# Optimization experiments

Hardware: AMD Instinct MI355X
Metric: run time of the kernel (lower is better)

The kernel has to match this reference:

```python
import jax, jax.numpy as jnp
import numpy as np

B, S, D = 4, 1024, 1024      # batch, seq_len, hidden_size
I = 4096                     # intermediate_size
E = 8                        # num_experts
K = 2                        # top-k


def setup_inputs() -> dict:
    key = jax.random.key(0)
    ks = jax.random.split(key, 8)
    x = jax.random.normal(ks[0], (B, S, D), dtype=jnp.float32)
    gate_w = jax.random.normal(ks[1], (E, D), dtype=jnp.float32) * 0.02
    gate_b = jnp.zeros((E,), dtype=jnp.float32)
    w1 = jax.random.normal(ks[2], (E, I, D), dtype=jnp.float32) * 0.02
    b1 = jnp.zeros((E, I), dtype=jnp.float32)
    w2 = jax.random.normal(ks[3], (E, D, I), dtype=jnp.float32) * 0.02
    b2 = jnp.zeros((E, D), dtype=jnp.float32)
    return {"x": x, "gate_w": gate_w, "gate_b": gate_b,
            "w1": w1, "b1": b1, "w2": w2, "b2": b2}


def reference(x, gate_w, gate_b, w1, b1, w2, b2):
    b, s, d = x.shape
    xf = x.reshape(-1, d)                                  # [N, D]
    logits = xf @ gate_w.T + gate_b                        # [N, E]
    top_vals, top_idx = jax.lax.top_k(logits, K)           # [N, K]
    top_w = jax.nn.softmax(top_vals, axis=-1)              # softmax over the k selected logits

    # combine[n, e] = routing weight of token n for expert e (0 if not selected)
    n_tok = xf.shape[0]
    combine = jnp.zeros((n_tok, w1.shape[0]), dtype=x.dtype)
    combine = combine.at[jnp.arange(n_tok)[:, None], top_idx].add(top_w)

    out = jnp.zeros_like(xf)
    for e in range(w1.shape[0]):                           # small fixed loop over experts
        h = jax.nn.gelu(xf @ w1[e].T + b1[e], approximate=False)  # exact GELU (torch default)
        out = out + combine[:, e:e + 1] * (h @ w2[e].T + b2[e])
    return out.reshape(b, s, d)
```

## Files before the change

### kernel.cpp

```cpp
#include <hip/hip_runtime.h>
#include <math.h>

#define NTOK 4096
#define DDIM 1024
#define IDIM 4096
#define NEXP 8
#define MAXPAD 9216

typedef _Float16 f16x8 __attribute__((ext_vector_type(8)));
typedef _Float16 f16x4 __attribute__((ext_vector_type(4)));
typedef float    f32x4 __attribute__((ext_vector_type(4)));

__device__ __forceinline__ void glds16(const _Float16* g, _Float16* l) {
    __builtin_amdgcn_global_load_lds(
        (const __attribute__((address_space(1))) _Float16*)g,
        (__attribute__((address_space(3))) _Float16*)l, 16, 0, 0);
}

__device__ __forceinline__ float fast_gelu(float v) {
    float u = v * (0.7978845608f + 0.0356774081f * v * v);
    float ex = __builtin_amdgcn_exp2f(u * 2.8853900817779268f);
    float th = 1.0f - 2.0f * __builtin_amdgcn_rcpf(ex + 1.0f);
    return 0.5f * v * (1.0f + th);
}

__global__ void cvt_kernel(const float* __restrict__ src, _Float16* __restrict__ dst, int n4) {
    int i = blockIdx.x * blockDim.x + threadIdx.x;
    if (i >= n4) return;
    float4 v = ((const float4*)src)[i];
    f16x4 o = { (_Float16)v.x, (_Float16)v.y, (_Float16)v.z, (_Float16)v.w };
    ((f16x4*)dst)[i] = o;
}

__global__ void gate_kernel(const float* __restrict__ x, const float* __restrict__ gw,
                            const float* __restrict__ gb,
                            int* __restrict__ cnt, int* __restrict__ tok,
                            float* __restrict__ wgt) {
    int wave = threadIdx.x >> 6;
    int lane = threadIdx.x & 63;
    int token = blockIdx.x * 4 + wave;
    const float* xr = x + (size_t)token * DDIM;
    float xv[16];
#pragma unroll
    for (int j = 0; j < 16; ++j) xv[j] = xr[lane + 64 * j];
    float lg[NEXP];
#pragma unroll
    for (int e = 0; e < NEXP; ++e) {
        const float* g = gw + e * DDIM;
        float s = 0.f;
#pragma unroll
        for (int j = 0; j < 16; ++j) s += xv[j] * g[lane + 64 * j];
#pragma unroll
        for (int o = 32; o > 0; o >>= 1) s += __shfl_xor(s, o, 64);
        lg[e] = s + gb[e];
    }
    if (lane == 0) {
        int i0 = 0; float v0 = lg[0];
        for (int e = 1; e < NEXP; ++e) if (lg[e] > v0) { v0 = lg[e]; i0 = e; }
        int i1 = -1; float v1 = -3.0e38f;
        for (int e = 0; e < NEXP; ++e) { if (e == i0) continue; if (lg[e] > v1) { v1 = lg[e]; i1 = e; } }
        float e1 = expf(v1 - v0);
        float den = 1.f + e1;
        float w0 = 1.f / den;
        float w1 = e1 / den;
        int p0 = atomicAdd(&cnt[i0], 1);
        tok[i0 * NTOK + p0] = token; wgt[i0 * NTOK + p0] = w0;
        int p1 = atomicAdd(&cnt[i1], 1);
        tok[i1 * NTOK + p1] = token; wgt[i1 * NTOK + p1] = w1;
    }
}

__global__ void scan_kernel(const int* __restrict__ cnt, int* __restrict__ off,
                            int* __restrict__ q1, int* __restrict__ q2) {
    if (threadIdx.x == 0) {
        int acc = 0;
        for (int e = 0; e < NEXP; ++e) { off[e] = acc; acc += ((cnt[e] + 127) >> 7) << 7; }
        off[NEXP] = acc;
        int n1 = 0, n2 = 0;
        for (int e = 0; e < NEXP; ++e) {
            int mtiles = (cnt[e] + 255) >> 8;
            for (int mt = 0; mt < mtiles; ++mt) {
                for (int nt = 0; nt < IDIM / 256; ++nt)
                    q1[n1++] = e | (mt << 4) | (nt << 12);
                for (int kc = 0; kc < 4; ++kc)
                    for (int nt = 0; nt < DDIM / 256; ++nt)
                        q2[n2++] = e | (mt << 4) | (nt << 12) | (kc << 20);
            }
        }
        off[10] = n1; off[11] = n2;
    }
}

__global__ void gather_kernel(const float* __restrict__ x, const int* __restrict__ cnt,
                              const int* __restrict__ off, const int* __restrict__ tok,
                              _Float16* __restrict__ xg) {
    int row = blockIdx.x;
    if (row >= off[NEXP]) return;
    int e = 0;
    while (e < NEXP - 1 && row >= off[e + 1]) ++e;
    int r = row - off[e];
    int t = threadIdx.x;
    _Float16* dst = xg + (size_t)row * DDIM;
    if (r < cnt[e]) {
        int token = tok[e * NTOK + r];
        float4 v = ((const float4*)(x + (size_t)token * DDIM))[t];
        f16x4 o = { (_Float16)v.x, (_Float16)v.y, (_Float16)v.z, (_Float16)v.w };
        ((f16x4*)dst)[t] = o;
    } else {
        f16x4 z = {};
        ((f16x4*)dst)[t] = z;
    }
}

#define SBAR() do { __builtin_amdgcn_s_barrier(); asm volatile("" ::: "memory"); } while (0)
#define STAGE(b, ko) do { \
    glds16(ap + (ko), &As[b][wv * 512]); \
    glds16(bp + (ko), &Bs[b][wv * 512]); \
} while (0)
#define ARD(buf, r) (*(const f16x8*)&As[buf][(r) * 32 + ((fq ^ (((r) >> 1) & 3)) << 3)])
#define BRD(buf, r) (*(const f16x8*)&Bs[buf][(r) * 32 + ((fq ^ (((r) >> 1) & 3)) << 3)])

template <int KDIM, int NDIM, int EPI, int SPLIT>
__global__ __launch_bounds__(1024, 4) void gemm256_kernel(
    const _Float16* __restrict__ A,
    const _Float16* __restrict__ Bw,
    const float* __restrict__ bias,
    const int* __restrict__ cnt, const int* __restrict__ off,
    const int* __restrict__ tok, const float* __restrict__ wgt,
    _Float16* __restrict__ Hout, float* __restrict__ Out,
    const int* __restrict__ qarr, const int* __restrict__ qn) {
    constexpr int KB = KDIM / SPLIT;
    constexpr int NK = KB / 32;

    __shared__ __align__(16) _Float16 As[4][256 * 32];
    __shared__ __align__(16) _Float16 Bs[4][256 * 32];

    const int tid = threadIdx.x;
    const int wv = tid >> 6, lane = tid & 63;
    const int wm = (wv >> 2) * 64;
    const int wn = (wv & 3) * 64;
    const int fr = lane & 15, fq = lane >> 4;
    const int srow = lane >> 2;
    const int scol = ((lane & 3) ^ ((lane >> 3) & 3)) << 3;
    const int nwork = *qn;

    for (int wi = blockIdx.x; wi < nwork; wi += gridDim.x) {
        __syncthreads();
        const int w = qarr[wi];
        const int e  = w & 15;
        const int mt = (w >> 4) & 255;
        const int nt = (w >> 12) & 255;
        const int kc = (w >> 20) & 7;
        const int ce = cnt[e];
        const int rowbase = off[e] + mt * 256;
        const int colbase = nt * 256;

        int ra = rowbase + wv * 16 + srow;
        if (ra > MAXPAD - 1) ra = MAXPAD - 1;
        const _Float16* ap = A + (size_t)ra * KDIM + kc * KB + scol;
        const _Float16* bp = Bw + ((size_t)e * NDIM + colbase + wv * 16 + srow) * KDIM + kc * KB + scol;

        f32x4 acc[4][4] = {};

        STAGE(0, 0); STAGE(1, 32); STAGE(2, 64);

        for (int kt = 0; kt < NK; ++kt) {
            const int buf = kt & 3;
            if (kt + 3 < NK) STAGE((kt + 3) & 3, (kt + 3) * 32);
            const int ahead = (NK - 1 - kt) < 3 ? (NK - 1 - kt) : 3;
            if (ahead == 3)      asm volatile("s_waitcnt vmcnt(6)" ::: "memory");
            else if (ahead == 2) asm volatile("s_waitcnt vmcnt(4)" ::: "memory");
            else if (ahead == 1) asm volatile("s_waitcnt vmcnt(2)" ::: "memory");
            else                 asm volatile("s_waitcnt vmcnt(0)" ::: "memory");
            SBAR();
            f16x8 a[4], b[4];
#pragma unroll
            for (int i = 0; i < 4; ++i) a[i] = ARD(buf, wm + i * 16 + fr);
#pragma unroll
            for (int j = 0; j < 4; ++j) b[j] = BRD(buf, wn + j * 16 + fr);
            __builtin_amdgcn_s_setprio(1);
#pragma unroll
            for (int i = 0; i < 4; ++i)
#pragma unroll
                for (int j = 0; j < 4; ++j)
                    acc[i][j] = __builtin_amdgcn_mfma_f32_16x16x32_f16(a[i], b[j], acc[i][j], 0, 0, 0);
            __builtin_amdgcn_s_setprio(0);
            asm volatile("s_waitcnt lgkmcnt(0)" ::: "memory");
            SBAR();
        }

        const int rq = fq << 2;
        if constexpr (EPI == 1) {
            const int elim = off[e + 1];
#pragma unroll
            for (int i = 0; i < 4; ++i) {
#pragma unroll
                for (int r = 0; r < 4; ++r) {
                    const int grow = rowbase + wm + i * 16 + rq + r;
                    if (grow < elim) {
#pragma unroll
                        for (int j = 0; j < 4; ++j) {
                            const int col = colbase + wn + j * 16 + fr;
                            float v = fast_gelu(acc[i][j][r] + bias[e * NDIM + col]);
                            Hout[(size_t)grow * NDIM + col] = (_Float16)v;
                        }
                    }
                }
            }
        } else {
#pragma unroll
            for (int i = 0; i < 4; ++i) {
#pragma unroll
                for (int r = 0; r < 4; ++r) {
                    const int slot = mt * 256 + wm + i * 16 + rq + r;
                    if (slot < ce) {
                        const int token = tok[e * NTOK + slot];
                        const float ww = wgt[e * NTOK + slot];
#pragma unroll
                        for (int j = 0; j < 4; ++j) {
                            const int col = colbase + wn + j * 16 + fr;
                            float v = acc[i][j][r];
                            if (kc == 0) v += bias[e * NDIM + col];
                            unsafeAtomicAdd(&Out[(size_t)token * NDIM + col], ww * v);
                        }
                    }
                }
            }
        }
    }
}

extern "C" void kernel_launch(void* const* d_in, const int* in_sizes, int n_in,
                              void* d_out, int out_size, void* d_ws, size_t ws_size,
                              hipStream_t stream) {
    const float* x      = (const float*)d_in[0];
    const float* gate_w = (const float*)d_in[1];
    const float* gate_b = (const float*)d_in[2];
    const float* w1     = (const float*)d_in[3];
    const float* b1     = (const float*)d_in[4];
    const float* w2     = (const float*)d_in[5];
    const float* b2     = (const float*)d_in[6];
    float* out = (float*)d_out;

    char* p = (char*)d_ws;
    _Float16* w1h  = (_Float16*)p; p += (size_t)NEXP * IDIM * DDIM * 2;
    _Float16* w2h  = (_Float16*)p; p += (size_t)NEXP * DDIM * IDIM * 2;
    _Float16* xg   = (_Float16*)p; p += (size_t)MAXPAD * DDIM * 2;
    _Float16* hbuf = (_Float16*)p; p += (size_t)MAXPAD * IDIM * 2;
    int*      tok  = (int*)p;      p += (size_t)NEXP * NTOK * 4;
    float*    wgt  = (float*)p;    p += (size_t)NEXP * NTOK * 4;
    int*      cnt  = (int*)p;      p += 128;
    int*      off  = (int*)p;      p += 128;
    int*      q1   = (int*)p;      p += 4096;
    int*      q2   = (int*)p;      p += 4096;

    hipMemsetAsync(cnt, 0, 128, stream);
    hipMemsetAsync(out, 0, (size_t)NTOK * DDIM * 4, stream);

    cvt_kernel<<<32768, 256, 0, stream>>>(w2, w2h, NEXP * DDIM * IDIM / 4);
    cvt_kernel<<<32768, 256, 0, stream>>>(w1, w1h, NEXP * IDIM * DDIM / 4);
    gate_kernel<<<NTOK / 4, 256, 0, stream>>>(x, gate_w, gate_b, cnt, tok, wgt);
    scan_kernel<<<1, 64, 0, stream>>>(cnt, off, q1, q2);
    gather_kernel<<<MAXPAD, 256, 0, stream>>>(x, cnt, off, tok, xg);

    gemm256_kernel<DDIM, IDIM, 1, 1><<<dim3(256), 1024, 0, stream>>>(
        xg, w1h, b1, cnt, off, tok, wgt, hbuf, (float*)nullptr, q1, off + 10);
    gemm256_kernel<IDIM, DDIM, 2, 4><<<dim3(256), 1024, 0, stream>>>(
        hbuf, w2h, b2, cnt, off, tok, wgt, (_Float16*)nullptr, out, q2, off + 11);
}
```

Before: 781.0 us.

## Shrink GEMM tiles to 128x256 with 512-thread blocks and double buffering

```diff
diff --git a/kernel.cpp b/kernel.cpp
--- a/kernel.cpp
+++ b/kernel.cpp
@@ -78,7 +78,7 @@
         off[NEXP] = acc;
         int n1 = 0, n2 = 0;
         for (int e = 0; e < NEXP; ++e) {
-            int mtiles = (cnt[e] + 255) >> 8;
+            int mtiles = (cnt[e] + 127) >> 7;
             for (int mt = 0; mt < mtiles; ++mt) {
                 for (int nt = 0; nt < IDIM / 256; ++nt)
                     q1[n1++] = e | (mt << 4) | (nt << 12);
@@ -112,16 +112,16 @@
     }
 }
 
-#define SBAR() do { __builtin_amdgcn_s_barrier(); asm volatile("" ::: "memory"); } while (0)
 #define STAGE(b, ko) do { \
-    glds16(ap + (ko), &As[b][wv * 512]); \
-    glds16(bp + (ko), &Bs[b][wv * 512]); \
+    glds16(gp0 + (ko), &Sh[b][lo0]); \
+    glds16(gp1 + (ko), &Sh[b][lo1]); \
+    glds16(gp2 + (ko), &Sh[b][lo2]); \
 } while (0)
-#define ARD(buf, r) (*(const f16x8*)&As[buf][(r) * 32 + ((fq ^ (((r) >> 1) & 3)) << 3)])
-#define BRD(buf, r) (*(const f16x8*)&Bs[buf][(r) * 32 + ((fq ^ (((r) >> 1) & 3)) << 3)])
+#define ARD(buf, r) (*(const f16x8*)&Sh[buf][(r) * 32 + ((fq ^ (((r) >> 1) & 3)) << 3)])
+#define BRD(buf, r) (*(const f16x8*)&Sh[buf][4096 + (r) * 32 + ((fq ^ (((r) >> 1) & 3)) << 3)])
 
 template <int KDIM, int NDIM, int EPI, int SPLIT>
-__global__ __launch_bounds__(1024, 4) void gemm256_kernel(
+__global__ __launch_bounds__(512, 4) void gemm256_kernel(
     const _Float16* __restrict__ A,
     const _Float16* __restrict__ Bw,
     const float* __restrict__ bias,
@@ -132,8 +132,7 @@
     constexpr int KB = KDIM / SPLIT;
     constexpr int NK = KB / 32;
 
-    __shared__ __align__(16) _Float16 As[4][256 * 32];
-    __shared__ __align__(16) _Float16 Bs[4][256 * 32];
+    __shared__ __align__(16) _Float16 Sh[2][384 * 32];
 
     const int tid = threadIdx.x;
     const int wv = tid >> 6, lane = tid & 63;
@@ -148,36 +147,49 @@
         __syncthreads();
         const int w = qarr[wi];
         const int e  = w & 15;
-        const int mt = (w >> 4) & 255;
-        const int nt = (w >> 12) & 255;
+        const int mt = (w >> 4) & 63;
+        const int nt = (w >> 12) & 31;
         const int kc = (w >> 20) & 7;
         const int ce = cnt[e];
-        const int rowbase = off[e] + mt * 256;
+        const int rowbase = off[e] + mt * 128;
         const int colbase = nt * 256;
 
-        int ra = rowbase + wv * 16 + srow;
-        if (ra > MAXPAD - 1) ra = MAXPAD - 1;
-        const _Float16* ap = A + (size_t)ra * KDIM + kc * KB + scol;
-        const _Float16* bp = Bw + ((size_t)e * NDIM + colbase + wv * 16 + srow) * KDIM + kc * KB + scol;
+        const int id0 = wv * 3, id1 = wv * 3 + 1, id2 = wv * 3 + 2;
+        const _Float16* gp0; const _Float16* gp1; const _Float16* gp2;
+        int lo0, lo1, lo2;
+        {
+            const _Float16* Ab = A + (size_t)rowbase * KDIM + kc * KB + scol;
+            const _Float16* Bb = Bw + ((size_t)e * NDIM + colbase) * KDIM + kc * KB + scol;
+            gp0 = (id0 < 8) ? Ab + (size_t)(id0 * 16 + srow) * KDIM
+                            : Bb + (size_t)((id0 - 8) * 16 + srow) * KDIM;
+            gp1 = (id1 < 8) ? Ab + (size_t)(id1 * 16 + srow) * KDIM
+                            : Bb + (size_t)((id1 - 8) * 16 + srow) * KDIM;
+            gp2 = Bb + (size_t)((id2 - 8) * 16 + srow) * KDIM;
+            if (id2 < 8) gp2 = Ab + (size_t)(id2 * 16 + srow) * KDIM;
+            lo0 = (id0 < 8) ? id0 * 512 : 4096 + (id0 - 8) * 512;
+            lo1 = (id1 < 8) ? id1 * 512 : 4096 + (id1 - 8) * 512;
+            lo2 = (id2 < 8) ? id2 * 512 : 4096 + (id2 - 8) * 512;
+        }
 
         f32x4 acc[4][4] = {};
 
-        STAGE(0, 0); STAGE(1, 32); STAGE(2, 64);
+        STAGE(0, 0);
 
         for (int kt = 0; kt < NK; ++kt) {
-            const int buf = kt & 3;
-            if (kt + 3 < NK) STAGE((kt + 3) & 3, (kt + 3) * 32);
-            const int ahead = (NK - 1 - kt) < 3 ? (NK - 1 - kt) : 3;
-            if (ahead == 3)      asm volatile("s_waitcnt vmcnt(6)" ::: "memory");
-            else if (ahead == 2) asm volatile("s_waitcnt vmcnt(4)" ::: "memory");
-            else if (ahead == 1) asm volatile("s_waitcnt vmcnt(2)" ::: "memory");
-            else                 asm volatile("s_waitcnt vmcnt(0)" ::: "memory");
-            SBAR();
+            const int cur = kt & 1, nxt = cur ^ 1;
+            if (kt + 1 < NK) {
+                STAGE(nxt, (kt + 1) * 32);
+                asm volatile("s_waitcnt vmcnt(3)");
+            } else {
+                asm volatile("s_waitcnt vmcnt(0)");
+            }
+            __builtin_amdgcn_s_barrier();
+            __builtin_amdgcn_sched_barrier(0);
             f16x8 a[4], b[4];
 #pragma unroll
-            for (int i = 0; i < 4; ++i) a[i] = ARD(buf, wm + i * 16 + fr);
-#pragma unroll
-            for (int j = 0; j < 4; ++j) b[j] = BRD(buf, wn + j * 16 + fr);
+            for (int i = 0; i < 4; ++i) a[i] = ARD(cur, wm + i * 16 + fr);
+#pragma unroll
+            for (int j = 0; j < 4; ++j) b[j] = BRD(cur, wn + j * 16 + fr);
             __builtin_amdgcn_s_setprio(1);
 #pragma unroll
             for (int i = 0; i < 4; ++i)
@@ -185,25 +197,23 @@
                 for (int j = 0; j < 4; ++j)
                     acc[i][j] = __builtin_amdgcn_mfma_f32_16x16x32_f16(a[i], b[j], acc[i][j], 0, 0, 0);
             __builtin_amdgcn_s_setprio(0);
-            asm volatile("s_waitcnt lgkmcnt(0)" ::: "memory");
-            SBAR();
+            __builtin_amdgcn_sched_barrier(0);
+            asm volatile("s_waitcnt lgkmcnt(0)");
+            __builtin_amdgcn_s_barrier();
         }
 
         const int rq = fq << 2;
         if constexpr (EPI == 1) {
-            const int elim = off[e + 1];
 #pragma unroll
             for (int i = 0; i < 4; ++i) {
 #pragma unroll
                 for (int r = 0; r < 4; ++r) {
                     const int grow = rowbase + wm + i * 16 + rq + r;
-                    if (grow < elim) {
-#pragma unroll
-                        for (int j = 0; j < 4; ++j) {
-                            const int col = colbase + wn + j * 16 + fr;
-                            float v = fast_gelu(acc[i][j][r] + bias[e * NDIM + col]);
-                            Hout[(size_t)grow * NDIM + col] = (_Float16)v;
-                        }
+#pragma unroll
+                    for (int j = 0; j < 4; ++j) {
+                        const int col = colbase + wn + j * 16 + fr;
+                        float v = fast_gelu(acc[i][j][r] + bias[e * NDIM + col]);
+                        Hout[(size_t)grow * NDIM + col] = (_Float16)v;
                     }
                 }
             }
@@ -212,7 +222,7 @@
             for (int i = 0; i < 4; ++i) {
 #pragma unroll
                 for (int r = 0; r < 4; ++r) {
-                    const int slot = mt * 256 + wm + i * 16 + rq + r;
+                    const int slot = mt * 128 + wm + i * 16 + rq + r;
                     if (slot < ce) {
                         const int token = tok[e * NTOK + slot];
                         const float ww = wgt[e * NTOK + slot];
@@ -251,8 +261,8 @@
     float*    wgt  = (float*)p;    p += (size_t)NEXP * NTOK * 4;
     int*      cnt  = (int*)p;      p += 128;
     int*      off  = (int*)p;      p += 128;
-    int*      q1   = (int*)p;      p += 4096;
-    int*      q2   = (int*)p;      p += 4096;
+    int*      q1   = (int*)p;      p += 8192;
+    int*      q2   = (int*)p;      p += 8192;
 
     hipMemsetAsync(cnt, 0, 128, stream);
     hipMemsetAsync(out, 0, (size_t)NTOK * DDIM * 4, stream);
@@ -263,8 +273,8 @@
     scan_kernel<<<1, 64, 0, stream>>>(cnt, off, q1, q2);
     gather_kernel<<<MAXPAD, 256, 0, stream>>>(x, cnt, off, tok, xg);
 
-    gemm256_kernel<DDIM, IDIM, 1, 1><<<dim3(256), 1024, 0, stream>>>(
+    gemm256_kernel<DDIM, IDIM, 1, 1><<<dim3(512), 512, 0, stream>>>(
         xg, w1h, b1, cnt, off, tok, wgt, hbuf, (float*)nullptr, q1, off + 10);
-    gemm256_kernel<IDIM, DDIM, 2, 4><<<dim3(256), 1024, 0, stream>>>(
+    gemm256_kernel<IDIM, DDIM, 2, 4><<<dim3(512), 512, 0, stream>>>(
         hbuf, w2h, b2, cnt, off, tok, wgt, (_Float16*)nullptr, out, q2, off + 11);
 }
```

Result: faster. 723.8 us (-7.3%).
